# Performance work log

Measured on AMD Instinct MI355X. Metric: run time of the kernel, lower is better.

Reference implementation:

```python
import jax, jax.numpy as jnp
import numpy as np
from jax import lax

EPS = 1e-4  # BatchNorm2d eps
K, STRIDE, PAD = 3, 1, 1


def _conv_nchw(x, w, stride, pad):
    return lax.conv_general_dilated(
        x, w, window_strides=(stride, stride), padding=[(pad, pad), (pad, pad)],
        dimension_numbers=("NCHW", "OIHW", "NCHW"))


def setup_inputs() -> dict:
    key = jax.random.key(0)
    ks = jax.random.split(key, 6)
    N, C, H, W = 16, 256, 56, 56
    Cout = 256
    return {
        "x": jax.random.normal(ks[0], (N, C, H, W), jnp.float32),
        "bn_gamma": jax.random.uniform(ks[1], (C,), jnp.float32, 0.5, 1.5),
        "bn_beta": jax.random.normal(ks[2], (C,), jnp.float32) * 0.1,
        "conv_w": jax.random.normal(ks[3], (Cout, C, K, K), jnp.float32) * (1.0 / np.sqrt(C * K * K)),
        "conv_b": jax.random.normal(ks[4], (Cout,), jnp.float32) * 0.01,
        "beta_conv_b": jax.random.normal(ks[5], (1,), jnp.float32) * 0.01,
    }


def reference(x, bn_gamma, bn_beta, conv_w, conv_b, beta_conv_b):
    # --- BatchNorm2d (training-mode batch stats, affine) ---
    mean = jnp.mean(x, axis=(0, 2, 3), keepdims=True)
    var = jnp.mean(jnp.square(x - mean), axis=(0, 2, 3), keepdims=True)  # biased
    xn = (x - mean) * lax.rsqrt(var + EPS)
    xn = xn * bn_gamma[None, :, None, None] + bn_beta[None, :, None, None]

    # --- Ternary quantize (threshold=0; le overwrites ge, so x==0 -> -1) ---
    t = jnp.where(xn >= 0.0, 1.0, 0.0)
    t = jnp.where(xn <= 0.0, -1.0, t).astype(xn.dtype)
    # scale=True, clamp=True
    xc = jnp.clip(xn, -1.0, 1.0)
    c_sum = jnp.sum(xc * t, axis=1, keepdims=True)       # [N,1,H,W]
    c_cnt = jnp.sum(jnp.abs(t), axis=1, keepdims=True)   # L1 norm over channels

    # --- Main conv on ternary activations ---
    y = _conv_nchw(t, conv_w, STRIDE, PAD) + conv_b[None, :, None, None]

    # --- beta: ones-weight box filter (+ beta_conv bias) ---
    ones_k = jnp.ones((1, 1, K, K), x.dtype)
    b_sum = _conv_nchw(c_sum, ones_k, STRIDE, PAD) + beta_conv_b[0]
    b_cnt = _conv_nchw(c_cnt, ones_k, STRIDE, PAD) + beta_conv_b[0]
    beta_map = b_sum / b_cnt                             # [N,1,Ho,Wo]
    return y * beta_map
```

## Files before the change

kernel.cpp:

```cpp
#include <hip/hip_runtime.h>
#include <hip/hip_bf16.h>

typedef __attribute__((ext_vector_type(8))) short bf16x8;
typedef __attribute__((ext_vector_type(4))) float f32x4;

#define NB 16
#define C 256
#define HH 56
#define WW 56
#define HW 3136
#define CHW 802816
#define NPIX 50176
#define PH 58
#define PW 58
#define KTOT 2304
#define PPI 3364
#define NPIXP 53824

#define GLL(g, l) __builtin_amdgcn_global_load_lds( \
    (const __attribute__((address_space(1))) void*)(g), \
    (__attribute__((address_space(3))) void*)(l), 16, 0, 0)

__global__ __launch_bounds__(1024) void prep_stats_kernel(const float* __restrict__ x,
                             const float* __restrict__ gamma, const float* __restrict__ cw,
                             double* __restrict__ stats, unsigned short* __restrict__ Wp,
                             unsigned short* __restrict__ Tp, float* __restrict__ csum) {
  int b = blockIdx.x, tid = threadIdx.x;
  if (b < 256) {
    int c = b;
    double s = 0.0, s2 = 0.0;
    const float* xc = x + (size_t)c * HW;
    for (int k = tid; k < NB * (HW / 4); k += 1024) {
      int n = k / (HW / 4), i = k - n * (HW / 4);
      float4 v = *(const float4*)(xc + (size_t)n * CHW + i * 4);
      double a = v.x, bb = v.y, cc = v.z, d = v.w;
      s  += (a + bb) + (cc + d);
      s2 += (a * a + bb * bb) + (cc * cc + d * d);
    }
    __shared__ double rs[1024], rq[1024];
    rs[tid] = s; rq[tid] = s2; __syncthreads();
    for (int o = 512; o > 0; o >>= 1) {
      if (tid < o) { rs[tid] += rs[tid + o]; rq[tid] += rq[tid + o]; }
      __syncthreads();
    }
    if (tid == 0) {
      double mean = rs[0] / (double)NPIX;
      double var = rq[0] / (double)NPIX - mean * mean;
      stats[c] = mean;
      stats[C + c] = (double)gamma[c] / sqrt(var + 1e-4);
    }
  } else if (b < 320) {
    int co = (b - 256) * 4 + (tid >> 8);
    int c  = tid & 255;
    const float* src = cw + (size_t)co * KTOT + c * 9;
    unsigned short* dst = Wp + (size_t)co * KTOT;
    int p = (c & 31) * 8 + (c >> 5);
#pragma unroll
    for (int t9 = 0; t9 < 9; ++t9) {
      unsigned u = __builtin_bit_cast(unsigned, src[t9]);
      unsigned lsb = (u >> 16) & 1u;
      u += 0x7FFFu + lsb;
      dst[t9 * 256 + p] = (unsigned short)(u >> 16);
    }
  } else if (b < 434) {
    int g = (b - 320) * 1024 + tid;
    int n = g / 7296; int r = g - n * 7296;
    int pix = r >> 5, c8 = r & 31;
    int h, w;
    if (pix < 58)      { h = 0;  w = pix; }
    else if (pix < 116){ h = 57; w = pix - 58; }
    else { int rem = pix - 116; h = 1 + (rem >> 1); w = (rem & 1) ? 57 : 0; }
    uint4 z = {0u, 0u, 0u, 0u};
    *(uint4*)(Tp + (size_t)((n * PH + h) * PW + w) * C + c8 * 8) = z;
  } else {
    int i = (b - 434) * 1024 + tid;
    if (i < NPIXP) csum[i] = 0.f;
  }
}

__global__ __launch_bounds__(256) void ternarize_kernel(const float* __restrict__ x,
                                 const float* __restrict__ beta,
                                 const double* __restrict__ stats,
                                 unsigned short* __restrict__ Tp, float* __restrict__ csum) {
  int bid = blockIdx.x, tid = threadIdx.x;
  int n = bid / HH, h = bid - n * HH;
  __shared__ float xs[256][57];
  const float* xb = x + (size_t)n * CHW + h * WW;
#pragma unroll
  for (int j = 0; j < 14; ++j) {
    int idx = j * 256 + tid;
    int c = idx / 14, q = idx - c * 14;
    float4 v = *(const float4*)(xb + (size_t)c * HW + q * 4);
    float* row = &xs[c][q * 4];
    row[0] = v.x; row[1] = v.y; row[2] = v.z; row[3] = v.w;
  }
  int c8 = tid & 31;
  double mu[8], sc[8], bt[8];
#pragma unroll
  for (int e = 0; e < 8; ++e) {
    int c = c8 + 32 * e;
    mu[e] = stats[c]; sc[e] = stats[C + c]; bt[e] = (double)beta[c];
  }
  __syncthreads();
  unsigned short* tb = Tp + ((size_t)(n * PH + h + 1) * PW + 1) * C;
  float* cs = csum + (size_t)(n * PH + h + 1) * PW + 1;
#pragma unroll
  for (int p = 0; p < 7; ++p) {
    int idx = p * 256 + tid;
    int w = idx >> 5;
    unsigned bits[4];
    float msum = 0.f;
#pragma unroll
    for (int e2 = 0; e2 < 4; ++e2) {
      unsigned lo, hi;
      {
        double xn = ((double)xs[c8 + 64 * e2][w] - mu[2 * e2]) * sc[2 * e2] + bt[2 * e2];
        lo = (xn > 0.0) ? 0x3F80u : 0xBF80u;
        msum += (float)fmin(fabs(xn), 1.0);
      }
      {
        double xn = ((double)xs[c8 + 64 * e2 + 32][w] - mu[2 * e2 + 1]) * sc[2 * e2 + 1] + bt[2 * e2 + 1];
        hi = (xn > 0.0) ? 0x3F80u : 0xBF80u;
        msum += (float)fmin(fabs(xn), 1.0);
      }
      bits[e2] = lo | (hi << 16);
    }
    msum += __shfl_xor(msum, 1); msum += __shfl_xor(msum, 2);
    msum += __shfl_xor(msum, 4); msum += __shfl_xor(msum, 8);
    msum += __shfl_xor(msum, 16);
    uint4 v4; v4.x = bits[0]; v4.y = bits[1]; v4.z = bits[2]; v4.w = bits[3];
    *(uint4*)(tb + (size_t)w * C + c8 * 8) = v4;
    if (c8 == 0) cs[w] = msum;
  }
}

__global__ __launch_bounds__(256) void conv_kernel(const unsigned short* __restrict__ Wp,
    const unsigned short* __restrict__ Tp, const float* __restrict__ convb,
    const float* __restrict__ csum, const float* __restrict__ betab,
    float* __restrict__ out) {
  int bid = blockIdx.x;
  int ptg = bid >> 5, xcd = bid & 7, ct = (bid >> 3) & 3;
  int pt = ptg * 8 + xcd;
  if (pt >= 211) return;
  int tid = threadIdx.x;
  int co0 = ct * 64;

  __shared__ __align__(16) unsigned short As[2][3 * 64 * 32];
  __shared__ __align__(16) unsigned short Bs[2][320 * 32];

  int aofs[3];
#pragma unroll
  for (int r = 0; r < 3; ++r) {
    int lin = r * 256 + tid;
    int co = (lin >> 2) & 63, tap3 = lin >> 8, pseg = lin & 3;
    int lseg = pseg ^ ((co >> 1) & 3);
    aofs[r] = (co0 + co) * KTOT + tap3 * 256 + lseg * 8;
  }
  int bpix[5], blseg[5];
#pragma unroll
  for (int r = 0; r < 5; ++r) {
    int lin = r * 256 + tid;
    bpix[r] = lin >> 2;
    blseg[r] = (lin & 3) ^ ((bpix[r] >> 1) & 3);
  }

  int lane = tid & 63, wid = tid >> 6;
  int quad = lane >> 4, row16 = lane & 15;
  int aFoff = row16 * 32 + (quad ^ ((row16 >> 1) & 3)) * 8;
  int jbase = wid * 64 + row16 + 31;

  f32x4 acc[4][4];
#pragma unroll
  for (int mi = 0; mi < 4; ++mi)
#pragma unroll
    for (int ni = 0; ni < 4; ++ni)
      acc[mi][ni] = (f32x4){0.f, 0.f, 0.f, 0.f};

  {
    int wbase = pt * 256 - 58 - 32;
#pragma unroll
    for (int r = 0; r < 3; ++r) GLL(Wp + aofs[r], &As[0][(r * 256 + tid) * 8]);
#pragma unroll
    for (int r = 0; r < 5; ++r) {
      int q = wbase + bpix[r];
      q = q < 0 ? 0 : (q >= NPIXP ? NPIXP - 1 : q);
      GLL(Tp + (size_t)q * C + blseg[r] * 8, &Bs[0][(r * 256 + tid) * 8]);
    }
  }

  for (int s = 0; s < 24; ++s) {
    int cur = s & 1;
    __syncthreads();
    if (s < 23) {
      int s2 = s + 1;
      int kh2 = s2 >> 3, c2 = (s2 & 7) * 32;
      int ao = kh2 * 768 + c2;
#pragma unroll
      for (int r = 0; r < 3; ++r) GLL(Wp + aofs[r] + ao, &As[cur ^ 1][(r * 256 + tid) * 8]);
      int wbase2 = pt * 256 + (kh2 - 1) * 58 - 32;
#pragma unroll
      for (int r = 0; r < 5; ++r) {
        int q = wbase2 + bpix[r];
        q = q < 0 ? 0 : (q >= NPIXP ? NPIXP - 1 : q);
        GLL(Tp + (size_t)q * C + blseg[r] * 8 + c2, &Bs[cur ^ 1][(r * 256 + tid) * 8]);
      }
    }
    const unsigned short* aB = &As[cur][0];
    const unsigned short* bB = &Bs[cur][0];
    __builtin_amdgcn_s_setprio(1);
#pragma unroll
    for (int kw = 0; kw < 3; ++kw) {
      bf16x8 a[4], b[4];
#pragma unroll
      for (int mi = 0; mi < 4; ++mi)
        a[mi] = *(const bf16x8*)(aB + kw * 2048 + mi * 512 + aFoff);
#pragma unroll
      for (int ni = 0; ni < 4; ++ni) {
        int pix = jbase + ni * 16 + kw;
        b[ni] = *(const bf16x8*)(bB + pix * 32 + ((quad ^ ((pix >> 1) & 3)) * 8));
      }
#pragma unroll
      for (int mi = 0; mi < 4; ++mi)
#pragma unroll
        for (int ni = 0; ni < 4; ++ni)
          acc[mi][ni] = __builtin_amdgcn_mfma_f32_16x16x32_bf16(a[mi], b[ni], acc[mi][ni], 0, 0, 0);
    }
    __builtin_amdgcn_s_setprio(0);
  }

  float bb = betab[0];
#pragma unroll
  for (int ni = 0; ni < 4; ++ni) {
    int pp = pt * 256 + wid * 64 + ni * 16 + row16;
    if (pp >= NPIXP) continue;
    int n = pp / PPI; int r2 = pp - n * PPI;
    int ph = r2 / PW;  int pw = r2 - ph * PW;
    if (ph < 1 || ph > 56 || pw < 1 || pw > 56) continue;
    const float* cp = csum + (size_t)(n * PH + ph - 1) * PW + (pw - 1);
    float s9 = 0.f;
#pragma unroll
    for (int i = 0; i < 3; ++i)
#pragma unroll
      for (int j = 0; j < 3; ++j) s9 += cp[i * PW + j];
    int rows = 3 - (ph == 1) - (ph == 56);
    int cols = 3 - (pw == 1) - (pw == 56);
    float bm = (s9 + bb) / (256.0f * (float)(rows * cols) + bb);
    int pix = (ph - 1) * WW + (pw - 1);
    float* ob = out + (size_t)n * CHW + pix;
#pragma unroll
    for (int mi = 0; mi < 4; ++mi) {
      int co = co0 + mi * 16 + quad * 4;
#pragma unroll
      for (int rg = 0; rg < 4; ++rg) {
        ob[(size_t)(co + rg) * HW] = (acc[mi][ni][rg] + convb[co + rg]) * bm;
      }
    }
  }
}

extern "C" void kernel_launch(void* const* d_in, const int* in_sizes, int n_in,
                              void* d_out, int out_size, void* d_ws, size_t ws_size,
                              hipStream_t stream) {
  const float* x     = (const float*)d_in[0];
  const float* gamma = (const float*)d_in[1];
  const float* beta  = (const float*)d_in[2];
  const float* convw = (const float*)d_in[3];
  const float* convb = (const float*)d_in[4];
  const float* betab = (const float*)d_in[5];
  float* out = (float*)d_out;

  char* ws = (char*)d_ws;
  unsigned short* Tp   = (unsigned short*)(ws);
  unsigned short* Wp   = (unsigned short*)(ws + 27557888);
  float*          csum = (float*)(ws + 28737536);
  double*         stats= (double*)(ws + 29153536);

  prep_stats_kernel<<<487, 1024, 0, stream>>>(x, gamma, convw, stats, Wp, Tp, csum);
  ternarize_kernel<<<896, 256, 0, stream>>>(x, beta, stats, Tp, csum);
  conv_kernel<<<864, 256, 0, stream>>>(Wp, Tp, convb, csum, betab, out);
}
```

Baseline: 201.9 us.

## Load conv weights directly from global in MFMA fragment layout, reuse input rows across kh

The weight repack now writes weights pre-swizzled into the per-lane MFMA fragment order, so the conv kernel reads A fragments straight from global/L2 instead of staging them through LDS. The B tile is enlarged to 384 pixels so it covers all three kernel rows, which cuts the K loop from 24 stages to 8 channel chunks and lets each staged input tile serve all 9 taps. Launch bounds request 2 blocks per SM. In exchange, weight fragment loads hit global memory inside the inner loop, which raises register pressure and adds global latency.

```diff
diff --git a/kernel.cpp b/kernel.cpp
--- a/kernel.cpp
+++ b/kernel.cpp
@@ -53,14 +53,17 @@
     int co = (b - 256) * 4 + (tid >> 8);
     int c  = tid & 255;
     const float* src = cw + (size_t)co * KTOT + c * 9;
-    unsigned short* dst = Wp + (size_t)co * KTOT;
     int p = (c & 31) * 8 + (c >> 5);
-#pragma unroll
-    for (int t9 = 0; t9 < 9; ++t9) {
-      unsigned u = __builtin_bit_cast(unsigned, src[t9]);
+    int ck = p >> 5, v = p & 31;
+    int quad = v >> 3, j = v & 7;
+    int cb = co >> 4, row16 = co & 15;
+    int lane8 = (quad * 16 + row16) * 8 + j;
+#pragma unroll
+    for (int tap = 0; tap < 9; ++tap) {
+      unsigned u = __builtin_bit_cast(unsigned, src[tap]);
       unsigned lsb = (u >> 16) & 1u;
       u += 0x7FFFu + lsb;
-      dst[t9 * 256 + p] = (unsigned short)(u >> 16);
+      Wp[(size_t)(((ck * 9 + tap) * 16) + cb) * 512 + lane8] = (unsigned short)(u >> 16);
     }
   } else if (b < 434) {
     int g = (b - 320) * 1024 + tid;
@@ -134,7 +137,7 @@
   }
 }
 
-__global__ __launch_bounds__(256) void conv_kernel(const unsigned short* __restrict__ Wp,
+__global__ __launch_bounds__(256, 2) void conv_kernel(const unsigned short* __restrict__ Wp,
     const unsigned short* __restrict__ Tp, const float* __restrict__ convb,
     const float* __restrict__ csum, const float* __restrict__ betab,
     float* __restrict__ out) {
@@ -143,31 +146,27 @@
   int pt = ptg * 8 + xcd;
   if (pt >= 211) return;
   int tid = threadIdx.x;
-  int co0 = ct * 64;
-
-  __shared__ __align__(16) unsigned short As[2][3 * 64 * 32];
-  __shared__ __align__(16) unsigned short Bs[2][320 * 32];
-
-  int aofs[3];
-#pragma unroll
-  for (int r = 0; r < 3; ++r) {
+
+  __shared__ __align__(16) unsigned short Bs[2][384 * 32];
+
+  int wstart = pt * 256 - 59;
+  int bofs[6];
+#pragma unroll
+  for (int r = 0; r < 6; ++r) {
     int lin = r * 256 + tid;
-    int co = (lin >> 2) & 63, tap3 = lin >> 8, pseg = lin & 3;
-    int lseg = pseg ^ ((co >> 1) & 3);
-    aofs[r] = (co0 + co) * KTOT + tap3 * 256 + lseg * 8;
-  }
-  int bpix[5], blseg[5];
-#pragma unroll
-  for (int r = 0; r < 5; ++r) {
-    int lin = r * 256 + tid;
-    bpix[r] = lin >> 2;
-    blseg[r] = (lin & 3) ^ ((bpix[r] >> 1) & 3);
+    int bpix = lin >> 2, pseg = lin & 3;
+    int lseg = pseg ^ ((bpix >> 1) & 3);
+    int q = wstart + bpix;
+    q = q < 0 ? 0 : (q >= NPIXP ? NPIXP - 1 : q);
+    bofs[r] = q * C + lseg * 8;
   }
 
   int lane = tid & 63, wid = tid >> 6;
   int quad = lane >> 4, row16 = lane & 15;
-  int aFoff = row16 * 32 + (quad ^ ((row16 >> 1) & 3)) * 8;
-  int jbase = wid * 64 + row16 + 31;
+  int pixb = wid * 64 + row16;
+
+  const bf16x8* Ab = (const bf16x8*)Wp + lane;
+  int cb0 = ct * 4;
 
   f32x4 acc[4][4];
 #pragma unroll
@@ -176,58 +175,46 @@
     for (int ni = 0; ni < 4; ++ni)
       acc[mi][ni] = (f32x4){0.f, 0.f, 0.f, 0.f};
 
-  {
-    int wbase = pt * 256 - 58 - 32;
-#pragma unroll
-    for (int r = 0; r < 3; ++r) GLL(Wp + aofs[r], &As[0][(r * 256 + tid) * 8]);
-#pragma unroll
-    for (int r = 0; r < 5; ++r) {
-      int q = wbase + bpix[r];
-      q = q < 0 ? 0 : (q >= NPIXP ? NPIXP - 1 : q);
-      GLL(Tp + (size_t)q * C + blseg[r] * 8, &Bs[0][(r * 256 + tid) * 8]);
-    }
-  }
-
-  for (int s = 0; s < 24; ++s) {
-    int cur = s & 1;
+#pragma unroll
+  for (int r = 0; r < 6; ++r) GLL(Tp + bofs[r], &Bs[0][(r * 256 + tid) * 8]);
+
+  for (int ck = 0; ck < 8; ++ck) {
+    int cur = ck & 1;
     __syncthreads();
-    if (s < 23) {
-      int s2 = s + 1;
-      int kh2 = s2 >> 3, c2 = (s2 & 7) * 32;
-      int ao = kh2 * 768 + c2;
-#pragma unroll
-      for (int r = 0; r < 3; ++r) GLL(Wp + aofs[r] + ao, &As[cur ^ 1][(r * 256 + tid) * 8]);
-      int wbase2 = pt * 256 + (kh2 - 1) * 58 - 32;
-#pragma unroll
-      for (int r = 0; r < 5; ++r) {
-        int q = wbase2 + bpix[r];
-        q = q < 0 ? 0 : (q >= NPIXP ? NPIXP - 1 : q);
-        GLL(Tp + (size_t)q * C + blseg[r] * 8 + c2, &Bs[cur ^ 1][(r * 256 + tid) * 8]);
-      }
-    }
-    const unsigned short* aB = &As[cur][0];
+    if (ck < 7) {
+      int c2 = (ck + 1) * 32;
+#pragma unroll
+      for (int r = 0; r < 6; ++r) GLL(Tp + bofs[r] + c2, &Bs[cur ^ 1][(r * 256 + tid) * 8]);
+    }
     const unsigned short* bB = &Bs[cur][0];
     __builtin_amdgcn_s_setprio(1);
 #pragma unroll
-    for (int kw = 0; kw < 3; ++kw) {
-      bf16x8 a[4], b[4];
-#pragma unroll
-      for (int mi = 0; mi < 4; ++mi)
-        a[mi] = *(const bf16x8*)(aB + kw * 2048 + mi * 512 + aFoff);
-#pragma unroll
-      for (int ni = 0; ni < 4; ++ni) {
-        int pix = jbase + ni * 16 + kw;
-        b[ni] = *(const bf16x8*)(bB + pix * 32 + ((quad ^ ((pix >> 1) & 3)) * 8));
-      }
-#pragma unroll
-      for (int mi = 0; mi < 4; ++mi)
-#pragma unroll
-        for (int ni = 0; ni < 4; ++ni)
-          acc[mi][ni] = __builtin_amdgcn_mfma_f32_16x16x32_bf16(a[mi], b[ni], acc[mi][ni], 0, 0, 0);
+    for (int kh = 0; kh < 3; ++kh) {
+      bf16x8 a[3][4];
+#pragma unroll
+      for (int kw = 0; kw < 3; ++kw)
+#pragma unroll
+        for (int mi = 0; mi < 4; ++mi)
+          a[kw][mi] = Ab[(size_t)(((ck * 9 + kh * 3 + kw) * 16) + cb0 + mi) * 64];
+#pragma unroll
+      for (int kw = 0; kw < 3; ++kw) {
+        bf16x8 b[4];
+#pragma unroll
+        for (int ni = 0; ni < 4; ++ni) {
+          int pix = pixb + ni * 16 + kh * 58 + kw;
+          b[ni] = *(const bf16x8*)(bB + pix * 32 + ((quad ^ ((pix >> 1) & 3)) * 8));
+        }
+#pragma unroll
+        for (int mi = 0; mi < 4; ++mi)
+#pragma unroll
+          for (int ni = 0; ni < 4; ++ni)
+            acc[mi][ni] = __builtin_amdgcn_mfma_f32_16x16x32_bf16(a[kw][mi], b[ni], acc[mi][ni], 0, 0, 0);
+      }
     }
     __builtin_amdgcn_s_setprio(0);
   }
 
+  int co0 = ct * 64;
   float bb = betab[0];
 #pragma unroll
   for (int ni = 0; ni < 4; ++ni) {
```

New measurement: 233.9 us. 15.9% more time.

## Enlarge conv tile to 512 pixels with triple-buffered LDS and interleaved prefetch

Applied to the files above, without the earlier changes.

The conv kernel now uses 512-thread blocks covering 512 padded pixels per tile (8 waves), halving the grid. A double-buffered A/B LDS pair is replaced by a single triple-buffered region with prefetch two stages ahead, explicit vmcnt waits and a raw s_barrier in place of __syncthreads. Global-to-LDS loads are spread across the kw MFMA sub-steps. This aims to hide load latency and amortize weight loads over more pixels, but it raises LDS use to about 144KB per block, which may limit occupancy, and makes the tail blocks coarser.

```diff
diff --git a/kernel.cpp b/kernel.cpp
--- a/kernel.cpp
+++ b/kernel.cpp
@@ -134,40 +134,48 @@
   }
 }
 
-__global__ __launch_bounds__(256) void conv_kernel(const unsigned short* __restrict__ Wp,
+__global__ __launch_bounds__(512, 2) void conv_kernel(const unsigned short* __restrict__ Wp,
     const unsigned short* __restrict__ Tp, const float* __restrict__ convb,
     const float* __restrict__ csum, const float* __restrict__ betab,
     float* __restrict__ out) {
   int bid = blockIdx.x;
   int ptg = bid >> 5, xcd = bid & 7, ct = (bid >> 3) & 3;
   int pt = ptg * 8 + xcd;
-  if (pt >= 211) return;
+  if (pt >= 106) return;
   int tid = threadIdx.x;
   int co0 = ct * 64;
 
-  __shared__ __align__(16) unsigned short As[2][3 * 64 * 32];
-  __shared__ __align__(16) unsigned short Bs[2][320 * 32];
-
-  int aofs[3];
-#pragma unroll
-  for (int r = 0; r < 3; ++r) {
-    int lin = r * 256 + tid;
-    int co = (lin >> 2) & 63, tap3 = lin >> 8, pseg = lin & 3;
-    int lseg = pseg ^ ((co >> 1) & 3);
-    aofs[r] = (co0 + co) * KTOT + tap3 * 256 + lseg * 8;
-  }
-  int bpix[5], blseg[5];
-#pragma unroll
-  for (int r = 0; r < 5; ++r) {
-    int lin = r * 256 + tid;
-    bpix[r] = lin >> 2;
-    blseg[r] = (lin & 3) ^ ((bpix[r] >> 1) & 3);
+  __shared__ __align__(16) unsigned short lds[3 * 24576];
+
+  int ofs[6][3];
+  const unsigned short* base1 = Wp;
+#pragma unroll
+  for (int r = 0; r < 6; ++r) {
+    int lin = r * 512 + tid;
+    if (lin < 768) {
+      int co = (lin >> 2) & 63, tap3 = lin >> 8, pseg = lin & 3;
+      int lseg = pseg ^ ((co >> 1) & 3);
+      int ab = (co0 + co) * KTOT + tap3 * 256 + lseg * 8;
+#pragma unroll
+      for (int kh = 0; kh < 3; ++kh) ofs[r][kh] = ab + kh * 768;
+    } else {
+      int lb = lin - 768;
+      int brow = lb >> 2, bseg = lb & 3;
+      int lseg = bseg ^ ((brow >> 1) & 3);
+#pragma unroll
+      for (int kh = 0; kh < 3; ++kh) {
+        int q = pt * 512 + (kh - 1) * 58 - 32 + brow;
+        q = q < 0 ? 0 : (q >= NPIXP ? NPIXP - 1 : q);
+        ofs[r][kh] = q * C + lseg * 8;
+      }
+      if (r == 1) base1 = Tp;
+    }
   }
 
   int lane = tid & 63, wid = tid >> 6;
   int quad = lane >> 4, row16 = lane & 15;
   int aFoff = row16 * 32 + (quad ^ ((row16 >> 1) & 3)) * 8;
-  int jbase = wid * 64 + row16 + 31;
+  int pixb = wid * 64 + row16;
 
   f32x4 acc[4][4];
 #pragma unroll
@@ -177,61 +185,64 @@
       acc[mi][ni] = (f32x4){0.f, 0.f, 0.f, 0.f};
 
   {
-    int wbase = pt * 256 - 58 - 32;
-#pragma unroll
-    for (int r = 0; r < 3; ++r) GLL(Wp + aofs[r], &As[0][(r * 256 + tid) * 8]);
-#pragma unroll
-    for (int r = 0; r < 5; ++r) {
-      int q = wbase + bpix[r];
-      q = q < 0 ? 0 : (q >= NPIXP ? NPIXP - 1 : q);
-      GLL(Tp + (size_t)q * C + blseg[r] * 8, &Bs[0][(r * 256 + tid) * 8]);
-    }
+    unsigned short* d0 = lds + tid * 8;
+    GLL(Wp    + ofs[0][0],      d0);
+    GLL(base1 + ofs[1][0],      d0 + 512 * 8);
+#pragma unroll
+    for (int r = 2; r < 6; ++r) GLL(Tp + ofs[r][0], d0 + r * 512 * 8);
+    unsigned short* d1 = lds + 24576 + tid * 8;
+    GLL(Wp    + ofs[0][0] + 32, d1);
+    GLL(base1 + ofs[1][0] + 32, d1 + 512 * 8);
+#pragma unroll
+    for (int r = 2; r < 6; ++r) GLL(Tp + ofs[r][0] + 32, d1 + r * 512 * 8);
   }
 
   for (int s = 0; s < 24; ++s) {
-    int cur = s & 1;
-    __syncthreads();
-    if (s < 23) {
-      int s2 = s + 1;
-      int kh2 = s2 >> 3, c2 = (s2 & 7) * 32;
-      int ao = kh2 * 768 + c2;
-#pragma unroll
-      for (int r = 0; r < 3; ++r) GLL(Wp + aofs[r] + ao, &As[cur ^ 1][(r * 256 + tid) * 8]);
-      int wbase2 = pt * 256 + (kh2 - 1) * 58 - 32;
-#pragma unroll
-      for (int r = 0; r < 5; ++r) {
-        int q = wbase2 + bpix[r];
-        q = q < 0 ? 0 : (q >= NPIXP ? NPIXP - 1 : q);
-        GLL(Tp + (size_t)q * C + blseg[r] * 8 + c2, &Bs[cur ^ 1][(r * 256 + tid) * 8]);
-      }
-    }
-    const unsigned short* aB = &As[cur][0];
-    const unsigned short* bB = &Bs[cur][0];
-    __builtin_amdgcn_s_setprio(1);
+    const unsigned short* buf = lds + (s % 3) * 24576;
+    unsigned short* pbuf = lds + ((s + 2) % 3) * 24576 + tid * 8;
+    int s2 = s + 2;
+    int kh2 = s2 >> 3, cof2 = (s2 & 7) * 32;
+    bool pref = s2 < 24;
+    if (s < 23) asm volatile("s_waitcnt vmcnt(6)" ::: "memory");
+    else        asm volatile("s_waitcnt vmcnt(0)" ::: "memory");
+    __builtin_amdgcn_s_barrier();
+    __builtin_amdgcn_sched_barrier(0);
+    const unsigned short* aF = buf + aFoff;
+    const unsigned short* bB = buf + 6144;
 #pragma unroll
     for (int kw = 0; kw < 3; ++kw) {
+      if (pref) {
+        if (kw == 0) {
+          GLL(Wp    + ofs[0][kh2] + cof2, pbuf);
+          GLL(base1 + ofs[1][kh2] + cof2, pbuf + 512 * 8);
+        } else {
+          GLL(Tp + ofs[2 * kw][kh2] + cof2,     pbuf + (2 * kw) * 512 * 8);
+          GLL(Tp + ofs[2 * kw + 1][kh2] + cof2, pbuf + (2 * kw + 1) * 512 * 8);
+        }
+      }
       bf16x8 a[4], b[4];
 #pragma unroll
       for (int mi = 0; mi < 4; ++mi)
-        a[mi] = *(const bf16x8*)(aB + kw * 2048 + mi * 512 + aFoff);
+        a[mi] = *(const bf16x8*)(aF + kw * 2048 + mi * 512);
 #pragma unroll
       for (int ni = 0; ni < 4; ++ni) {
-        int pix = jbase + ni * 16 + kw;
+        int pix = pixb + ni * 16 + kw + 31;
         b[ni] = *(const bf16x8*)(bB + pix * 32 + ((quad ^ ((pix >> 1) & 3)) * 8));
       }
+      __builtin_amdgcn_s_setprio(1);
 #pragma unroll
       for (int mi = 0; mi < 4; ++mi)
 #pragma unroll
         for (int ni = 0; ni < 4; ++ni)
           acc[mi][ni] = __builtin_amdgcn_mfma_f32_16x16x32_bf16(a[mi], b[ni], acc[mi][ni], 0, 0, 0);
-    }
-    __builtin_amdgcn_s_setprio(0);
+      __builtin_amdgcn_s_setprio(0);
+    }
   }
 
   float bb = betab[0];
 #pragma unroll
   for (int ni = 0; ni < 4; ++ni) {
-    int pp = pt * 256 + wid * 64 + ni * 16 + row16;
+    int pp = pt * 512 + wid * 64 + ni * 16 + row16;
     if (pp >= NPIXP) continue;
     int n = pp / PPI; int r2 = pp - n * PPI;
     int ph = r2 / PW;  int pw = r2 - ph * PW;
@@ -277,5 +288,5 @@
 
   prep_stats_kernel<<<487, 1024, 0, stream>>>(x, gamma, convw, stats, Wp, Tp, csum);
   ternarize_kernel<<<896, 256, 0, stream>>>(x, beta, stats, Tp, csum);
-  conv_kernel<<<864, 256, 0, stream>>>(Wp, Tp, convb, csum, betab, out);
-}
+  conv_kernel<<<448, 512, 0, stream>>>(Wp, Tp, convb, csum, betab, out);
+}
```

Result: faster. 197.5 us (-2.1%).
